# Kernel optimization log

Measured on AMD Instinct MI355X. Metric: run time of the kernel, lower is better.

The kernel has to match this reference:

```python
import jax, jax.numpy as jnp
import numpy as np

IN_FEATURES = 4096
OUT_FEATURES = 14336
TILE = 16
BITS = 3
HAD = 128  # Hadamard block size used by EXL3 rotations


def _hadamard_matrix(n):
    H = np.array([[1.0]], dtype=np.float64)
    while H.shape[0] < n:
        H = np.block([[H, H], [H, -H]])
    return H

H128 = jnp.asarray(_hadamard_matrix(HAD) / np.sqrt(HAD), dtype=jnp.float32)


def had128(v):
    # blockwise normalized Hadamard transform over the last axis
    s = v.shape
    return (v.reshape(s[:-1] + (s[-1] // HAD, HAD)) @ H128).reshape(s)


def dequant_trellis(trellis):
    # trellis: [Tk, Tn, 48] uint16. Each 16x16 tile holds 256 weights coded as a
    # tail-biting trellis bitstream of 256*3 = 768 bits (48 uint16 words).
    # Weight i's 16-bit state is the circular bit window [3i, 3i+16).
    u = trellis.astype(jnp.uint32)  # [Tk, Tn, 48]
    i = jnp.arange(TILE * TILE)  # 256 weights per tile
    b = i * BITS                 # bit offset of each state
    w = b // 16                  # word index
    r = (b % 16).astype(jnp.uint32)
    hi = u[..., w]               # [Tk, Tn, 256]
    lo = u[..., (w + 1) % 48]
    comb = (hi << 16) | lo       # 32-bit window starting at word w
    states = (comb >> (jnp.uint32(16) - r)) & jnp.uint32(0xFFFF)
    # QTIP-style 3INST decode: LCG, exponent mask, sum of two fp16 bitcasts
    z = states * jnp.uint32(89226354) + jnp.uint32(64248484)
    z = z & jnp.uint32(0x8FFF8FFF)
    lo16 = jax.lax.bitcast_convert_type((z & jnp.uint32(0xFFFF)).astype(jnp.uint16), jnp.float16)
    hi16 = jax.lax.bitcast_convert_type((z >> 16).astype(jnp.uint16), jnp.float16)
    vals = lo16.astype(jnp.float32) + hi16.astype(jnp.float32)  # [Tk, Tn, 256]
    Tk, Tn = trellis.shape[0], trellis.shape[1]
    W = vals.reshape(Tk, Tn, TILE, TILE).transpose(0, 2, 1, 3).reshape(Tk * TILE, Tn * TILE)
    return W  # [K, N] float32


def setup_inputs() -> dict:
    key = jax.random.key(0)
    k1, k2, k3, k4, k5 = jax.random.split(key, 5)
    x = jax.random.normal(k1, (8, IN_FEATURES), dtype=jnp.float16)
    trellis = jax.random.randint(
        k2, (IN_FEATURES // TILE, OUT_FEATURES // TILE, 48), 0, 65536, dtype=jnp.int32
    ).astype(jnp.uint16)
    suh = jax.random.normal(k3, (IN_FEATURES,), dtype=jnp.float16)
    svh = jax.random.normal(k4, (OUT_FEATURES,), dtype=jnp.float16)
    bias = (jax.random.normal(k5, (OUT_FEATURES,), dtype=jnp.float16) * jnp.float16(0.01))
    return {"x": x, "trellis": trellis, "suh": suh, "svh": svh, "bias": bias}


def reference(x, trellis, suh, svh, bias):
    # EXL3 linear: y = Had( Had(x * suh) @ Wq ) * svh + bias
    W = dequant_trellis(trellis)                       # [K, N]
    xs = x.astype(jnp.float32) * suh.astype(jnp.float32)
    xh = had128(xs)                                    # input rotation
    y = xh @ W                                         # [B, N]
    yh = had128(y)                                     # output rotation
    out = yh * svh.astype(jnp.float32) + bias.astype(jnp.float32)
    return out.astype(jnp.float16)
```

## Files before the change

### kernel.cpp

```cpp
#include <hip/hip_runtime.h>
#include <hip/hip_fp16.h>
#include <hip/hip_bf16.h>
#include <stdint.h>


#define IN_F 4096
#define OUT_F 14336
#define BATCH 8
#define TN_TILES 896
#define KSLICES 8
#define ITERS 16
#define RS128 0.08838834764831845f

typedef __attribute__((ext_vector_type(4))) float f32x4;
typedef __attribute__((ext_vector_type(8))) _Float16 f16x8;
typedef __attribute__((ext_vector_type(2))) unsigned short u16x2;

__device__ _Float16 g_xh[BATCH * IN_F];
__device__ float g_part[KSLICES * BATCH * OUT_F];

__global__ void k_rot_in(const void* __restrict__ xp,
                         const void* __restrict__ suhp) {
  const int b = blockIdx.x;
  const int row = b >> 5, blk = b & 31;
  const int lane = threadIdx.x;
  const uint32_t ffmt =
      __any((((const uint32_t*)xp)[lane] & 0x1FFFu) != 0) ? 0u : 1u;
  const int i0 = blk * 128 + lane;
  float x0, x1, s0, s1;
  if (ffmt) {
    const float* x = (const float*)xp;
    const float* sh = (const float*)suhp;
    x0 = x[row * IN_F + i0];      x1 = x[row * IN_F + i0 + 64];
    s0 = sh[i0];                  s1 = sh[i0 + 64];
  } else {
    const __hip_bfloat16* x = (const __hip_bfloat16*)xp;
    const __hip_bfloat16* sh = (const __hip_bfloat16*)suhp;
    x0 = __bfloat162float(x[row * IN_F + i0]);
    x1 = __bfloat162float(x[row * IN_F + i0 + 64]);
    s0 = __bfloat162float(sh[i0]);
    s1 = __bfloat162float(sh[i0 + 64]);
  }
  float v0 = x0 * s0 * RS128;
  float v1 = x1 * s1 * RS128;
  { float a = v0 + v1, s = v0 - v1; v0 = a; v1 = s; }
  #pragma unroll
  for (int d = 32; d >= 1; d >>= 1) {
    float w0 = __shfl_xor(v0, d);
    float w1 = __shfl_xor(v1, d);
    if (lane & d) { v0 = w0 - v0; v1 = w1 - v1; }
    else          { v0 = v0 + w0; v1 = v1 + w1; }
  }
  g_xh[row * IN_F + i0]      = (_Float16)v0;
  g_xh[row * IN_F + i0 + 64] = (_Float16)v1;
}

__global__ __launch_bounds__(256) void k_main(const uint32_t* __restrict__ tr) {
  __shared__ uint32_t cwin[4][32][48];
  const int t = threadIdx.x;
  const int lane = t & 63;
  const int wv = t >> 6;
  const int tn = blockIdx.x * 4 + wv;
  const int ks = blockIdx.y;
  const uint32_t fmt = __any((tr[lane] >> 16) != 0) ? 1u : 0u;

  const int tile = lane >> 1;
  const int h = lane & 1;
  uint32_t d[12];
  if (fmt) {
    const uint4* gp = (const uint4*)(tr +
        ((long)(ks * 32 + tile) * TN_TILES + tn) * 24 + h * 12);
    uint4 a0 = gp[0], a1 = gp[1], a2 = gp[2];
    d[0] = a0.x; d[1] = a0.y; d[2]  = a0.z; d[3]  = a0.w;
    d[4] = a1.x; d[5] = a1.y; d[6]  = a1.z; d[7]  = a1.w;
    d[8] = a2.x; d[9] = a2.y; d[10] = a2.z; d[11] = a2.w;
  } else {
    const uint4* gp = (const uint4*)(tr +
        ((long)(ks * 32 + tile) * TN_TILES + tn) * 48 + h * 24);
    uint4 b0 = gp[0], b1 = gp[1], b2 = gp[2];
    uint4 b3 = gp[3], b4 = gp[4], b5 = gp[5];
    d[0]  = __builtin_amdgcn_perm(b0.y, b0.x, 0x05040100u);
    d[1]  = __builtin_amdgcn_perm(b0.w, b0.z, 0x05040100u);
    d[2]  = __builtin_amdgcn_perm(b1.y, b1.x, 0x05040100u);
    d[3]  = __builtin_amdgcn_perm(b1.w, b1.z, 0x05040100u);
    d[4]  = __builtin_amdgcn_perm(b2.y, b2.x, 0x05040100u);
    d[5]  = __builtin_amdgcn_perm(b2.w, b2.z, 0x05040100u);
    d[6]  = __builtin_amdgcn_perm(b3.y, b3.x, 0x05040100u);
    d[7]  = __builtin_amdgcn_perm(b3.w, b3.z, 0x05040100u);
    d[8]  = __builtin_amdgcn_perm(b4.y, b4.x, 0x05040100u);
    d[9]  = __builtin_amdgcn_perm(b4.w, b4.z, 0x05040100u);
    d[10] = __builtin_amdgcn_perm(b5.y, b5.x, 0x05040100u);
    d[11] = __builtin_amdgcn_perm(b5.w, b5.z, 0x05040100u);
  }
  uint32_t dnext = __shfl(d[0], lane ^ 1, 64);
  uint32_t c[24];
  #pragma unroll
  for (int m = 0; m < 12; ++m) {
    uint32_t nx = (m < 11) ? d[m + 1] : dnext;
    c[2 * m]     = (d[m] >> 16) | (d[m] << 16);
    c[2 * m + 1] = __builtin_amdgcn_perm(d[m], nx, 0x07060100u);
  }
  {
    uint32_t* wp = &cwin[wv][tile][h * 24];
    #pragma unroll
    for (int k = 0; k < 6; ++k)
      *(uint4*)(wp + 4 * k) = *(const uint4*)(c + 4 * k);
  }

  const int q = lane >> 4;
  const int cc = lane & 15;
  const int par = q >> 1;
  const int w0 = 3 * ((q & 1) << 3) + ((3 * cc) >> 4);
  const uint32_t shr = 16u - (uint32_t)((3 * cc) & 15);
  const uint32_t* myc = &cwin[wv][par][w0];

  auto lds_fetch = [&](int it, uint32_t* dst) {
    const uint32_t* cb = myc + it * 96;
    #pragma unroll
    for (int g = 0; g < 4; ++g) {
      dst[2 * g]     = cb[6 * g];
      dst[2 * g + 1] = cb[6 * g + 3];
    }
  };
  auto a_fetch = [&](int it) -> f16x8 {
    f16x8 a = {0, 0, 0, 0, 0, 0, 0, 0};
    if (cc < 8)
      a = *(const f16x8*)(g_xh + cc * IN_F + ks * 512 + it * 32 + q * 8);
    return a;
  };

  f32x4 acc = {0.f, 0.f, 0.f, 0.f};
  uint32_t cwA[8];
  lds_fetch(0, cwA);
  f16x8 aA = a_fetch(0);

  #pragma unroll 4
  for (int it = 0; it < ITERS; ++it) {
    uint32_t cwN[8] = {0, 0, 0, 0, 0, 0, 0, 0};
    f16x8 aN = {0, 0, 0, 0, 0, 0, 0, 0};
    if (it + 1 < ITERS) {
      lds_fetch(it + 1, cwN);
      aN = a_fetch(it + 1);
    }

    union { __half2 h2[4]; f16x8 v; } bfrag;
    #pragma unroll
    for (int g = 0; g < 4; ++g) {
      uint32_t c0 = cwA[2 * g], c1 = cwA[2 * g + 1];
      uint32_t st0 = (c0 >> shr) & 0xFFFFu;
      uint32_t st1 = (c1 >> shr) & 0xFFFFu;
      uint32_t t0 = __umul24(st0, 31858u) + 64248484u;
      uint32_t t1 = __umul24(st1, 31858u) + 64248484u;
      union { uint32_t u; u16x2 v; } sp, pm, th;
      sp.u = __builtin_amdgcn_perm(st1, st0, 0x05040100u);
      pm.v = sp.v * (u16x2){1361, 1361};
      th.u = __builtin_amdgcn_perm(t1, t0, 0x07060302u);
      th.v = th.v + pm.v;
      uint32_t hi = th.u & 0x8FFF8FFFu;
      uint32_t lo = __builtin_amdgcn_perm(t1, t0, 0x05040100u) & 0x8FFF8FFFu;
      __half2 ha = *(__half2*)&lo;
      __half2 hb = *(__half2*)&hi;
      bfrag.h2[g] = __hadd2(ha, hb);
    }

    acc = __builtin_amdgcn_mfma_f32_16x16x32_f16(aA, bfrag.v, acc, 0, 0, 0);

    #pragma unroll
    for (int g = 0; g < 8; ++g) cwA[g] = cwN[g];
    aA = aN;
  }

  if (q < 2) {
    const int n = tn * 16 + cc;
    #pragma unroll
    for (int rg = 0; rg < 4; ++rg)
      g_part[((ks * BATCH) + q * 4 + rg) * OUT_F + n] = acc[rg];
  }
}

__global__ void k_rot_out(const void* __restrict__ xp,
                          const void* __restrict__ svhp,
                          const void* __restrict__ biasp,
                          void* __restrict__ outp) {
  const int nblk = blockIdx.x;
  const int row = blockIdx.y;
  const int lane = threadIdx.x;
  const uint32_t ffmt =
      __any((((const uint32_t*)xp)[lane] & 0x1FFFu) != 0) ? 0u : 1u;
  const int n0 = nblk * 128 + lane;
  float v0 = 0.f, v1 = 0.f;
  #pragma unroll
  for (int s = 0; s < KSLICES; ++s) {
    v0 += g_part[(s * BATCH + row) * OUT_F + n0];
    v1 += g_part[(s * BATCH + row) * OUT_F + n0 + 64];
  }
  v0 *= RS128; v1 *= RS128;
  { float a = v0 + v1, s = v0 - v1; v0 = a; v1 = s; }
  #pragma unroll
  for (int d = 32; d >= 1; d >>= 1) {
    float w0 = __shfl_xor(v0, d);
    float w1 = __shfl_xor(v1, d);
    if (lane & d) { v0 = w0 - v0; v1 = w1 - v1; }
    else          { v0 = v0 + w0; v1 = v1 + w1; }
  }
  if (ffmt) {
    const float* svh = (const float*)svhp;
    const float* bias = (const float*)biasp;
    float* out = (float*)outp;
    out[(long)row * OUT_F + n0]      = v0 * svh[n0] + bias[n0];
    out[(long)row * OUT_F + n0 + 64] = v1 * svh[n0 + 64] + bias[n0 + 64];
  } else {
    const __hip_bfloat16* svh = (const __hip_bfloat16*)svhp;
    const __hip_bfloat16* bias = (const __hip_bfloat16*)biasp;
    __hip_bfloat16* out = (__hip_bfloat16*)outp;
    out[(long)row * OUT_F + n0] = __float2bfloat16(
        v0 * __bfloat162float(svh[n0]) + __bfloat162float(bias[n0]));
    out[(long)row * OUT_F + n0 + 64] = __float2bfloat16(
        v1 * __bfloat162float(svh[n0 + 64]) + __bfloat162float(bias[n0 + 64]));
  }
}

extern "C" void kernel_launch(void* const* d_in, const int* in_sizes, int n_in,
                              void* d_out, int out_size, void* d_ws,
                              size_t ws_size, hipStream_t stream) {
  const void*     x    = d_in[0];
  const uint32_t* tr   = (const uint32_t*)d_in[1];
  const void*     suh  = d_in[2];
  const void*     svh  = d_in[3];
  const void*     bias = d_in[4];

  k_rot_in<<<256, 64, 0, stream>>>(x, suh);
  k_main<<<dim3(TN_TILES / 4, KSLICES), 256, 0, stream>>>(tr);
  k_rot_out<<<dim3(OUT_F / 128, BATCH), 64, 0, stream>>>(x, svh, bias, d_out);
}
```

Measured before the change: 103.9 us.

## Fuse input Hadamard rotation into main GEMV kernel via shared memory

Removes the separate k_rot_in launch. Each k_main block now computes the rotated activations for its own K-slice, storing them in a padded LDS buffer, and the MFMA A operand is read from LDS instead of from a global scratch array. This saves one kernel launch and the global round-trip for the rotated x. In exchange, all 224 blocks per K-slice redo the same rotation work, and a __syncthreads is added before the main loop.

```diff
diff --git a/kernel.cpp b/kernel.cpp
--- a/kernel.cpp
+++ b/kernel.cpp
@@ -10,59 +10,28 @@
 #define TN_TILES 896
 #define KSLICES 8
 #define ITERS 16
+#define XH_PAD 520
 #define RS128 0.08838834764831845f
 
 typedef __attribute__((ext_vector_type(4))) float f32x4;
 typedef __attribute__((ext_vector_type(8))) _Float16 f16x8;
 typedef __attribute__((ext_vector_type(2))) unsigned short u16x2;
 
-__device__ _Float16 g_xh[BATCH * IN_F];
 __device__ float g_part[KSLICES * BATCH * OUT_F];
 
-__global__ void k_rot_in(const void* __restrict__ xp,
-                         const void* __restrict__ suhp) {
-  const int b = blockIdx.x;
-  const int row = b >> 5, blk = b & 31;
-  const int lane = threadIdx.x;
-  const uint32_t ffmt =
-      __any((((const uint32_t*)xp)[lane] & 0x1FFFu) != 0) ? 0u : 1u;
-  const int i0 = blk * 128 + lane;
-  float x0, x1, s0, s1;
-  if (ffmt) {
-    const float* x = (const float*)xp;
-    const float* sh = (const float*)suhp;
-    x0 = x[row * IN_F + i0];      x1 = x[row * IN_F + i0 + 64];
-    s0 = sh[i0];                  s1 = sh[i0 + 64];
-  } else {
-    const __hip_bfloat16* x = (const __hip_bfloat16*)xp;
-    const __hip_bfloat16* sh = (const __hip_bfloat16*)suhp;
-    x0 = __bfloat162float(x[row * IN_F + i0]);
-    x1 = __bfloat162float(x[row * IN_F + i0 + 64]);
-    s0 = __bfloat162float(sh[i0]);
-    s1 = __bfloat162float(sh[i0 + 64]);
-  }
-  float v0 = x0 * s0 * RS128;
-  float v1 = x1 * s1 * RS128;
-  { float a = v0 + v1, s = v0 - v1; v0 = a; v1 = s; }
-  #pragma unroll
-  for (int d = 32; d >= 1; d >>= 1) {
-    float w0 = __shfl_xor(v0, d);
-    float w1 = __shfl_xor(v1, d);
-    if (lane & d) { v0 = w0 - v0; v1 = w1 - v1; }
-    else          { v0 = v0 + w0; v1 = v1 + w1; }
-  }
-  g_xh[row * IN_F + i0]      = (_Float16)v0;
-  g_xh[row * IN_F + i0 + 64] = (_Float16)v1;
-}
-
-__global__ __launch_bounds__(256) void k_main(const uint32_t* __restrict__ tr) {
+__global__ __launch_bounds__(256) void k_main(const uint32_t* __restrict__ tr,
+                                              const void* __restrict__ xp,
+                                              const void* __restrict__ suhp) {
   __shared__ uint32_t cwin[4][32][48];
+  __shared__ _Float16 xh_s[BATCH][XH_PAD];
   const int t = threadIdx.x;
   const int lane = t & 63;
   const int wv = t >> 6;
   const int tn = blockIdx.x * 4 + wv;
   const int ks = blockIdx.y;
   const uint32_t fmt = __any((tr[lane] >> 16) != 0) ? 1u : 0u;
+  const uint32_t ffmt =
+      __any((((const uint32_t*)xp)[lane] & 0x1FFFu) != 0) ? 0u : 1u;
 
   const int tile = lane >> 1;
   const int h = lane & 1;
@@ -92,6 +61,40 @@
     d[10] = __builtin_amdgcn_perm(b5.y, b5.x, 0x05040100u);
     d[11] = __builtin_amdgcn_perm(b5.w, b5.z, 0x05040100u);
   }
+
+  #pragma unroll
+  for (int uu = 0; uu < 8; ++uu) {
+    const int row = 2 * wv + (uu >> 2);
+    const int hb = uu & 3;
+    const int col = ks * 512 + hb * 128 + lane;
+    float x0, x1, s0, s1;
+    if (ffmt) {
+      const float* xx = (const float*)xp;
+      const float* sh = (const float*)suhp;
+      x0 = xx[row * IN_F + col];      x1 = xx[row * IN_F + col + 64];
+      s0 = sh[col];                   s1 = sh[col + 64];
+    } else {
+      const __hip_bfloat16* xx = (const __hip_bfloat16*)xp;
+      const __hip_bfloat16* sh = (const __hip_bfloat16*)suhp;
+      x0 = __bfloat162float(xx[row * IN_F + col]);
+      x1 = __bfloat162float(xx[row * IN_F + col + 64]);
+      s0 = __bfloat162float(sh[col]);
+      s1 = __bfloat162float(sh[col + 64]);
+    }
+    float v0 = x0 * s0 * RS128;
+    float v1 = x1 * s1 * RS128;
+    { float a = v0 + v1, s = v0 - v1; v0 = a; v1 = s; }
+    #pragma unroll
+    for (int dd = 32; dd >= 1; dd >>= 1) {
+      float w0 = __shfl_xor(v0, dd);
+      float w1 = __shfl_xor(v1, dd);
+      if (lane & dd) { v0 = w0 - v0; v1 = w1 - v1; }
+      else           { v0 = v0 + w0; v1 = v1 + w1; }
+    }
+    xh_s[row][hb * 128 + lane]      = (_Float16)v0;
+    xh_s[row][hb * 128 + lane + 64] = (_Float16)v1;
+  }
+
   uint32_t dnext = __shfl(d[0], lane ^ 1, 64);
   uint32_t c[24];
   #pragma unroll
@@ -106,6 +109,8 @@
     for (int k = 0; k < 6; ++k)
       *(uint4*)(wp + 4 * k) = *(const uint4*)(c + 4 * k);
   }
+
+  __syncthreads();
 
   const int q = lane >> 4;
   const int cc = lane & 15;
@@ -125,7 +130,7 @@
   auto a_fetch = [&](int it) -> f16x8 {
     f16x8 a = {0, 0, 0, 0, 0, 0, 0, 0};
     if (cc < 8)
-      a = *(const f16x8*)(g_xh + cc * IN_F + ks * 512 + it * 32 + q * 8);
+      a = *(const f16x8*)(&xh_s[cc][it * 32 + q * 8]);
     return a;
   };
 
@@ -229,7 +234,6 @@
   const void*     svh  = d_in[3];
   const void*     bias = d_in[4];
 
-  k_rot_in<<<256, 64, 0, stream>>>(x, suh);
-  k_main<<<dim3(TN_TILES / 4, KSLICES), 256, 0, stream>>>(tr);
+  k_main<<<dim3(TN_TILES / 4, KSLICES), 256, 0, stream>>>(tr, x, suh);
   k_rot_out<<<dim3(OUT_F / 128, BATCH), 64, 0, stream>>>(x, svh, bias, d_out);
 }
```

Result: slower. 110.0 us (+5.8%).
